# Kernel optimization log

Measured on AMD Instinct MI355X. Metric: run time of the kernel, lower is better.

Reference implementation:

```python
import jax, jax.numpy as jnp
import numpy as np
from jax import lax

DIM = 64
HEADS = 4
B, Q, V = 8, 128, 128


def _modrelu(z, b):
    m = jnp.abs(z)
    return z * (jax.nn.relu(m + b) / (m + 1e-5))


def _eunn_unitary(h, th1, ph1, th2, ph2, om):
    # tunable-style EUNN, capacity 2: even-pair rotations, odd-pair rotations, diagonal phase
    d = h.shape[-1]
    # layer 1: pairs (0,1),(2,3),...
    hp = h.reshape(*h.shape[:-1], d // 2, 2)
    a, b = hp[..., 0], hp[..., 1]
    c1, s1, e1 = jnp.cos(th1), jnp.sin(th1), jnp.exp(1j * ph1)
    h = jnp.stack([e1 * (c1 * a - s1 * b), s1 * a + c1 * b], -1).reshape(h.shape)
    # layer 2: pairs (1,2),(3,4),...,(d-3,d-2); endpoints pass through
    mid = h[..., 1:d - 1].reshape(*h.shape[:-1], d // 2 - 1, 2)
    a, b = mid[..., 0], mid[..., 1]
    c2, s2, e2 = jnp.cos(th2), jnp.sin(th2), jnp.exp(1j * ph2)
    mid2 = jnp.stack([e2 * (c2 * a - s2 * b), s2 * a + c2 * b], -1).reshape(*h.shape[:-1], d - 2)
    h = jnp.concatenate([h[..., :1], mid2, h[..., d - 1:]], -1)
    return h * jnp.exp(1j * om)


def _forward(queries, values, U_re, U_im, bias, theta1, phi1, theta2, phi2, omega, W_dense, b_dense):
    Bq, Qq, d = queries.shape
    Vv = values.shape[1]
    # quadratic (query, value) expansion -> [B*Q, V, 2d]
    dq = jnp.broadcast_to(queries[:, :, None, :], (Bq, Qq, Vv, d))
    dv = jnp.broadcast_to(values[:, None, :, :], (Bq, Qq, Vv, d))
    x = jnp.concatenate([dq, dv], -1).reshape(Bq * Qq, Vv, 2 * d)
    U = (U_re + 1j * U_im)  # [H, 2d, d] complex input kernel per head
    Ux = jnp.einsum('nvi,hij->hvnj', x.astype(jnp.complex64), U)  # [H, V, N, d]

    def run_head(Ux_h, t1, p1, t2, p2, om, bh):
        def step(h, u):
            h2 = _modrelu(_eunn_unitary(h, t1, p1, t2, p2, om) + u, bh)
            return h2, None
        h0 = jnp.zeros(Ux_h.shape[1:], dtype=jnp.complex64)  # [N, d]
        hT, _ = lax.scan(step, h0, Ux_h)
        return hT  # final state, as Keras RNN with return_sequences=False

    outs = jax.vmap(run_head)(Ux, theta1, phi1, theta2, phi2, omega, bias)  # [H, N, d]
    acc = jnp.real(outs).transpose(1, 0, 2).reshape(Bq * Qq, HEADS * d)
    y = acc @ W_dense + b_dense
    return y.reshape(Bq, Qq, d)


def setup_inputs() -> dict:
    key = jax.random.key(0)
    ks = jax.random.split(key, 12)
    pi = np.pi
    return {
        'queries': jax.random.normal(ks[0], (B, Q, DIM), jnp.float32),
        'values': jax.random.normal(ks[1], (B, V, DIM), jnp.float32),
        'U_re': jax.random.normal(ks[2], (HEADS, 2 * DIM, DIM), jnp.float32) * (1.0 / np.sqrt(2 * DIM)),
        'U_im': jax.random.normal(ks[3], (HEADS, 2 * DIM, DIM), jnp.float32) * (1.0 / np.sqrt(2 * DIM)),
        'bias': jax.random.normal(ks[4], (HEADS, DIM), jnp.float32) * 0.01,
        'theta1': jax.random.uniform(ks[5], (HEADS, DIM // 2), jnp.float32, -pi, pi),
        'phi1': jax.random.uniform(ks[6], (HEADS, DIM // 2), jnp.float32, -pi, pi),
        'theta2': jax.random.uniform(ks[7], (HEADS, DIM // 2 - 1), jnp.float32, -pi, pi),
        'phi2': jax.random.uniform(ks[8], (HEADS, DIM // 2 - 1), jnp.float32, -pi, pi),
        'omega': jax.random.uniform(ks[9], (HEADS, DIM), jnp.float32, -pi, pi),
        'W_dense': jax.random.normal(ks[10], (HEADS * DIM, DIM), jnp.float32) * (1.0 / np.sqrt(HEADS * DIM)),
        'b_dense': jnp.zeros((DIM,), jnp.float32),
    }


def reference(queries, values, U_re, U_im, bias, theta1, phi1, theta2, phi2, omega, W_dense, b_dense):
    return _forward(queries, values, U_re, U_im, bias, theta1, phi1, theta2, phi2, omega, W_dense, b_dense)
```

## Files before the change

kernel.cpp:

```cpp
#include <hip/hip_runtime.h>
#include <math.h>

#define DIM 64
#define HEADS 4
#define BB 8
#define QQ 128
#define VV 128
#define NN (BB*QQ)

typedef float f2 __attribute__((ext_vector_type(2)));

__device__ __forceinline__ float dpp_swap1(float x) {
    return __int_as_float(__builtin_amdgcn_update_dpp(
        0, __float_as_int(x), 0xB1, 0xF, 0xF, true));
}
__device__ __forceinline__ float dpp_wshr1(float x) {
    return __int_as_float(__builtin_amdgcn_update_dpp(
        0, __float_as_int(x), 0x138, 0xF, 0xF, true));
}
__device__ __forceinline__ float dpp_wshl1(float x) {
    return __int_as_float(__builtin_amdgcn_update_dpp(
        0, __float_as_int(x), 0x130, 0xF, 0xF, true));
}
__device__ __forceinline__ f2 dpp2_swap1(f2 x) {
    f2 r; r.x = dpp_swap1(x.x); r.y = dpp_swap1(x.y); return r;
}
__device__ __forceinline__ f2 dpp2_shl1(f2 x) {
    f2 r; r.x = dpp_wshl1(x.x); r.y = dpp_wshl1(x.y); return r;
}
__device__ __forceinline__ f2 dpp2_shr1(f2 x) {
    f2 r; r.x = dpp_wshr1(x.x); r.y = dpp_wshr1(x.y); return r;
}

__global__ __launch_bounds__(256) void k_av(const float* __restrict__ values,
                                            const float* __restrict__ U_re,
                                            const float* __restrict__ U_im,
                                            f2* __restrict__ Av) {
    int tid = blockIdx.x * blockDim.x + threadIdx.x;
    int w = tid >> 6;
    int j = tid & 63;
    int h = w >> 8;
    int r0 = (w & 255) << 2;
    const float* vrow = values + r0 * DIM;
    const float* ur = U_re + (h * 2 * DIM + DIM) * DIM + j;
    const float* ui = U_im + (h * 2 * DIM + DIM) * DIM + j;
    f2 a0 = 0.f, a1 = 0.f, a2 = 0.f, a3 = 0.f;
    #pragma unroll 8
    for (int i = 0; i < DIM; ++i) {
        f2 u; u.x = ur[i * DIM]; u.y = ui[i * DIM];
        a0 += vrow[i] * u;
        a1 += vrow[DIM + i] * u;
        a2 += vrow[2 * DIM + i] * u;
        a3 += vrow[3 * DIM + i] * u;
    }
    f2* out = Av + (h * 1024 + r0) * DIM + j;
    out[0] = a0; out[DIM] = a1; out[2 * DIM] = a2; out[3 * DIM] = a3;
}

__global__ __launch_bounds__(256) void k_rnn_dense(
        const float* __restrict__ queries,
        const float* __restrict__ U_re,
        const float* __restrict__ U_im,
        const float* __restrict__ bias,
        const float* __restrict__ theta1,
        const float* __restrict__ phi1,
        const float* __restrict__ theta2,
        const float* __restrict__ phi2,
        const float* __restrict__ omega,
        const f2* __restrict__ Av,
        const float* __restrict__ W_dense,
        const float* __restrict__ b_dense,
        float* __restrict__ y) {
    int b = blockIdx.x >> 6;
    int q = blockIdx.x & 63;
    int t = threadIdx.x;
    int h = t >> 6;
    int j = t & 63;
    int n0 = b * 128 + q;
    int n1 = n0 + 64;

    int k1 = j >> 1;
    float th1 = theta1[h * 32 + k1], ph1 = phi1[h * 32 + k1];
    float c1 = cosf(th1), s1 = sinf(th1);
    float A1r, A1i, B1r, B1i;
    if ((j & 1) == 0) {
        float er = cosf(ph1), ei = sinf(ph1);
        A1r = er * c1; A1i = ei * c1;
        B1r = -er * s1; B1i = -ei * s1;
    } else {
        A1r = c1; A1i = 0.f;
        B1r = s1; B1i = 0.f;
    }

    float A2r, A2i, BLr, BLi, BRr, BRi;
    if (j == 0 || j == 63) {
        A2r = 1.f; A2i = 0.f; BLr = 0.f; BLi = 0.f; BRr = 0.f; BRi = 0.f;
    } else {
        int k2 = (j - 1) >> 1;
        float th2 = theta2[h * 31 + k2], ph2 = phi2[h * 31 + k2];
        float c2 = cosf(th2), s2 = sinf(th2);
        if (j & 1) {
            float er = cosf(ph2), ei = sinf(ph2);
            A2r = er * c2; A2i = ei * c2;
            BLr = -er * s2; BLi = -ei * s2;
            BRr = 0.f; BRi = 0.f;
        } else {
            A2r = c2; A2i = 0.f;
            BRr = s2; BRi = 0.f;
            BLr = 0.f; BLi = 0.f;
        }
    }
    {
        float om = omega[h * 64 + j];
        float eor = cosf(om), eoi = sinf(om);
        float tr, ti;
        tr = A2r * eor - A2i * eoi; ti = A2r * eoi + A2i * eor; A2r = tr; A2i = ti;
        tr = BLr * eor - BLi * eoi; ti = BLr * eoi + BLi * eor; BLr = tr; BLi = ti;
        tr = BRr * eor - BRi * eoi; ti = BRr * eoi + BRi * eor; BRr = tr; BRi = ti;
    }
    float bj = bias[h * 64 + j];

    const float* qrow0 = queries + n0 * DIM;
    const float* qrow1 = queries + n1 * DIM;
    const float* ur = U_re + (h * 2 * DIM) * DIM + j;
    const float* ui = U_im + (h * 2 * DIM) * DIM + j;
    f2 Uqr = 0.f, Uqi = 0.f;
    #pragma unroll 8
    for (int i = 0; i < DIM; ++i) {
        f2 a; a.x = qrow0[i]; a.y = qrow1[i];
        float wr = ur[i * DIM], wi = ui[i * DIM];
        Uqr += a * wr;
        Uqi += a * wi;
    }

    const f2* p = Av + (h * 1024 + b * 128) * DIM + j;

    f2 a0 = p[0], a1 = p[DIM], a2 = p[2 * DIM], a3 = p[3 * DIM];
    f2 Hr = 0.f, Hi = 0.f;
    f2 uvr = Uqr + a0.x, uvi = Uqi + a0.y;
    #pragma unroll 4
    for (int v = 0; v < VV; ++v) {
        f2 a4 = p[4 * DIM];
        p += DIM;
        f2 Pr = dpp2_swap1(Hr), Pi = dpp2_swap1(Hi);
        f2 Tr = (A1r * Hr - A1i * Hi) + (B1r * Pr - B1i * Pi);
        f2 Ti = (A1r * Hi + A1i * Hr) + (B1r * Pi + B1i * Pr);
        f2 Lr = dpp2_shl1(Tr), Li = dpp2_shl1(Ti);
        f2 Rr = dpp2_shr1(Tr), Ri = dpp2_shr1(Ti);
        f2 Sr = (A2r * Tr - A2i * Ti) + (BLr * Lr - BLi * Li) + (BRr * Rr - BRi * Ri);
        f2 Si = (A2r * Ti + A2i * Tr) + (BLr * Li + BLi * Lr) + (BRr * Ri + BRi * Rr);
        f2 Zr = Sr + uvr;
        f2 Zi = Si + uvi;
        uvr = Uqr + a1.x; uvi = Uqi + a1.y;
        a0 = a1; a1 = a2; a2 = a3; a3 = a4;
        f2 q2 = Zr * Zr + Zi * Zi + 1e-10f;
        f2 rs; rs.x = __builtin_amdgcn_rsqf(q2.x); rs.y = __builtin_amdgcn_rsqf(q2.y);
        f2 sc;
        sc.x = fmaxf(fmaf(bj, rs.x, 1.f), 0.f);
        sc.y = fmaxf(fmaf(bj, rs.y, 1.f), 0.f);
        Hr = Zr * sc; Hi = Zi * sc;
    }

    __shared__ float s_acc[2][HEADS * DIM];
    __shared__ float s_part[256];
    s_acc[0][h * 64 + j] = Hr.x;
    s_acc[1][h * 64 + j] = Hr.y;
    __syncthreads();

    {
        int r = t >> 7, hf = (t >> 6) & 1, jj = t & 63;
        const float* Wp = W_dense + (hf * 128) * DIM + jj;
        const float* ap = &s_acc[r][hf * 128];
        float part = 0.f;
        #pragma unroll 8
        for (int k = 0; k < 128; ++k)
            part = fmaf(ap[k], Wp[k * DIM], part);
        s_part[t] = part;
    }
    __syncthreads();
    if (t < 128) {
        int r = t >> 6, jj = t & 63;
        y[(n0 + r * 64) * DIM + jj] =
            b_dense[jj] + s_part[r * 128 + jj] + s_part[r * 128 + 64 + jj];
    }
}

extern "C" void kernel_launch(void* const* d_in, const int* in_sizes, int n_in,
                              void* d_out, int out_size, void* d_ws, size_t ws_size,
                              hipStream_t stream) {
    const float* queries = (const float*)d_in[0];
    const float* values  = (const float*)d_in[1];
    const float* U_re    = (const float*)d_in[2];
    const float* U_im    = (const float*)d_in[3];
    const float* bias    = (const float*)d_in[4];
    const float* theta1  = (const float*)d_in[5];
    const float* phi1    = (const float*)d_in[6];
    const float* theta2  = (const float*)d_in[7];
    const float* phi2    = (const float*)d_in[8];
    const float* omega   = (const float*)d_in[9];
    const float* W_dense = (const float*)d_in[10];
    const float* b_dense = (const float*)d_in[11];
    float* y = (float*)d_out;

    f2* Av = (f2*)d_ws;

    k_av<<<256, 256, 0, stream>>>(values, U_re, U_im, Av);
    k_rnn_dense<<<512, 256, 0, stream>>>(queries, U_re, U_im, bias, theta1,
                                         phi1, theta2, phi2, omega, Av,
                                         W_dense, b_dense, y);
}
```

Measured before the change: 119.5 us.

## Factor rotation coefficients into real rotation plus phase and batch-prefetch Av

Each step's complex coefficient multiplies are rewritten as a real cos/sin rotation followed by one complex phase multiply. This cuts the multiply count per recurrence step. The Av loads are also restructured into 8-deep register double-buffering, so global load latency is hidden behind 8 recurrence steps. The cost is extra register use and a reordered floating-point sum that may shift rounding slightly.

```diff
diff --git a/kernel.cpp b/kernel.cpp
--- a/kernel.cpp
+++ b/kernel.cpp
@@ -81,43 +81,35 @@
 
     int k1 = j >> 1;
     float th1 = theta1[h * 32 + k1], ph1 = phi1[h * 32 + k1];
-    float c1 = cosf(th1), s1 = sinf(th1);
-    float A1r, A1i, B1r, B1i;
+    float C1 = cosf(th1);
+    float s1v = sinf(th1);
+    float S1, E1r, E1i;
     if ((j & 1) == 0) {
-        float er = cosf(ph1), ei = sinf(ph1);
-        A1r = er * c1; A1i = ei * c1;
-        B1r = -er * s1; B1i = -ei * s1;
+        S1 = -s1v; E1r = cosf(ph1); E1i = sinf(ph1);
     } else {
-        A1r = c1; A1i = 0.f;
-        B1r = s1; B1i = 0.f;
-    }
-
-    float A2r, A2i, BLr, BLi, BRr, BRi;
+        S1 = s1v; E1r = 1.f; E1i = 0.f;
+    }
+
+    float C2, SL, SR, p2r, p2i;
     if (j == 0 || j == 63) {
-        A2r = 1.f; A2i = 0.f; BLr = 0.f; BLi = 0.f; BRr = 0.f; BRi = 0.f;
+        C2 = 1.f; SL = 0.f; SR = 0.f; p2r = 1.f; p2i = 0.f;
     } else {
         int k2 = (j - 1) >> 1;
         float th2 = theta2[h * 31 + k2], ph2 = phi2[h * 31 + k2];
         float c2 = cosf(th2), s2 = sinf(th2);
         if (j & 1) {
-            float er = cosf(ph2), ei = sinf(ph2);
-            A2r = er * c2; A2i = ei * c2;
-            BLr = -er * s2; BLi = -ei * s2;
-            BRr = 0.f; BRi = 0.f;
+            C2 = c2; SL = -s2; SR = 0.f;
+            p2r = cosf(ph2); p2i = sinf(ph2);
         } else {
-            A2r = c2; A2i = 0.f;
-            BRr = s2; BRi = 0.f;
-            BLr = 0.f; BLi = 0.f;
+            C2 = c2; SR = s2; SL = 0.f;
+            p2r = 1.f; p2i = 0.f;
         }
     }
-    {
-        float om = omega[h * 64 + j];
-        float eor = cosf(om), eoi = sinf(om);
-        float tr, ti;
-        tr = A2r * eor - A2i * eoi; ti = A2r * eoi + A2i * eor; A2r = tr; A2i = ti;
-        tr = BLr * eor - BLi * eoi; ti = BLr * eoi + BLi * eor; BLr = tr; BLi = ti;
-        tr = BRr * eor - BRi * eoi; ti = BRr * eoi + BRi * eor; BRr = tr; BRi = ti;
-    }
+    float om = omega[h * 64 + j];
+    float eor = cosf(om), eoi = sinf(om);
+    float PHr = p2r * eor - p2i * eoi;
+    float PHi = p2r * eoi + p2i * eor;
+
     float bj = bias[h * 64 + j];
 
     const float* qrow0 = queries + n0 * DIM;
@@ -135,30 +127,42 @@
 
     const f2* p = Av + (h * 1024 + b * 128) * DIM + j;
 
-    f2 a0 = p[0], a1 = p[DIM], a2 = p[2 * DIM], a3 = p[3 * DIM];
+    f2 buf[8], nxt[8];
+    #pragma unroll
+    for (int k = 0; k < 8; ++k) buf[k] = p[k * DIM];
+
     f2 Hr = 0.f, Hi = 0.f;
-    f2 uvr = Uqr + a0.x, uvi = Uqi + a0.y;
-    #pragma unroll 4
-    for (int v = 0; v < VV; ++v) {
-        f2 a4 = p[4 * DIM];
-        p += DIM;
-        f2 Pr = dpp2_swap1(Hr), Pi = dpp2_swap1(Hi);
-        f2 Tr = (A1r * Hr - A1i * Hi) + (B1r * Pr - B1i * Pi);
-        f2 Ti = (A1r * Hi + A1i * Hr) + (B1r * Pi + B1i * Pr);
-        f2 Lr = dpp2_shl1(Tr), Li = dpp2_shl1(Ti);
-        f2 Rr = dpp2_shr1(Tr), Ri = dpp2_shr1(Ti);
-        f2 Sr = (A2r * Tr - A2i * Ti) + (BLr * Lr - BLi * Li) + (BRr * Rr - BRi * Ri);
-        f2 Si = (A2r * Ti + A2i * Tr) + (BLr * Li + BLi * Lr) + (BRr * Ri + BRi * Rr);
-        f2 Zr = Sr + uvr;
-        f2 Zi = Si + uvi;
-        uvr = Uqr + a1.x; uvi = Uqi + a1.y;
-        a0 = a1; a1 = a2; a2 = a3; a3 = a4;
-        f2 q2 = Zr * Zr + Zi * Zi + 1e-10f;
-        f2 rs; rs.x = __builtin_amdgcn_rsqf(q2.x); rs.y = __builtin_amdgcn_rsqf(q2.y);
-        f2 sc;
-        sc.x = fmaxf(fmaf(bj, rs.x, 1.f), 0.f);
-        sc.y = fmaxf(fmaf(bj, rs.y, 1.f), 0.f);
-        Hr = Zr * sc; Hi = Zi * sc;
+    for (int vb = 0; vb < VV; vb += 8) {
+        const f2* pn = p + ((vb < VV - 8) ? 8 * DIM : 0);
+        #pragma unroll
+        for (int k = 0; k < 8; ++k) nxt[k] = pn[k * DIM];
+        p = pn;
+        #pragma unroll
+        for (int k = 0; k < 8; ++k) {
+            f2 av = buf[k];
+            f2 uvr = Uqr + av.x;
+            f2 uvi = Uqi + av.y;
+            f2 Pr = dpp2_swap1(Hr), Pi = dpp2_swap1(Hi);
+            f2 tpr = C1 * Hr + S1 * Pr;
+            f2 tpi = C1 * Hi + S1 * Pi;
+            f2 Tr = E1r * tpr - E1i * tpi;
+            f2 Ti = E1r * tpi + E1i * tpr;
+            f2 Lr = dpp2_shl1(Tr), Li = dpp2_shl1(Ti);
+            f2 Rr = dpp2_shr1(Tr), Ri = dpp2_shr1(Ti);
+            f2 spr = C2 * Tr + SL * Lr + SR * Rr;
+            f2 spi = C2 * Ti + SL * Li + SR * Ri;
+            f2 Zr = (PHr * spr - PHi * spi) + uvr;
+            f2 Zi = (PHr * spi + PHi * spr) + uvi;
+            f2 q2 = Zr * Zr + Zi * Zi + 1e-10f;
+            float rsx = __builtin_amdgcn_rsqf(q2.x);
+            float rsy = __builtin_amdgcn_rsqf(q2.y);
+            f2 sc;
+            sc.x = fmaxf(fmaf(bj, rsx, 1.f), 0.f);
+            sc.y = fmaxf(fmaf(bj, rsy, 1.f), 0.f);
+            Hr = Zr * sc; Hi = Zi * sc;
+        }
+        #pragma unroll
+        for (int k = 0; k < 8; ++k) buf[k] = nxt[k];
     }
 
     __shared__ float s_acc[2][HEADS * DIM];
```

Measured after the change: 117.3 us. About the same (-1.8%).
